# Optimization experiments

Hardware: AMD Instinct MI355X
Metric: run time of the kernel (lower is better)

## Reference

```python
import jax, jax.numpy as jnp
import numpy as np

D_MODEL, D_FF, RANK = 1024, 4096, 256
B, S = 4, 4096


def setup_inputs() -> dict:
    key = jax.random.key(0)
    ks = jax.random.split(key, 7)
    return {
        "x":  jax.random.normal(ks[0], (B, S, D_MODEL), dtype=jnp.float32),
        "U1": jax.random.normal(ks[1], (D_MODEL, RANK), dtype=jnp.float32) * 0.02,
        "V1": jax.random.normal(ks[2], (RANK, D_FF), dtype=jnp.float32) * 0.02,
        "b1": jnp.zeros((D_FF,), dtype=jnp.float32),
        "U2": jax.random.normal(ks[3], (D_FF, RANK), dtype=jnp.float32) * 0.02,
        "V2": jax.random.normal(ks[4], (RANK, D_MODEL), dtype=jnp.float32) * 0.02,
        "b2": jnp.zeros((D_MODEL,), dtype=jnp.float32),
    }


def reference(x, U1, V1, b1, U2, V2, b2):
    # P = x @ U1  -> low-rank projection [B, S, rank]
    P = jnp.einsum("bsd,dr->bsr", x, U1)
    # H = gelu(P @ V1 + b1)  -> [B, S, d_ff] (the intermediate the flash kernel tiles over)
    H = jax.nn.gelu(jnp.einsum("bsr,rf->bsf", P, V1) + b1)
    # Q = H @ U2 -> [B, S, rank]; out = Q @ V2 + b2 -> [B, S, d_model]
    Q = jnp.einsum("bsf,fr->bsr", H, U2)
    return jnp.einsum("bsr,rd->bsd", Q, V2) + b2
```

## Files before the change

### kernel.cpp

```cpp
#include <hip/hip_runtime.h>
#include <hip/hip_bf16.h>


typedef __attribute__((ext_vector_type(8))) short bfrag8;
typedef __attribute__((ext_vector_type(4))) float fx4;
typedef __attribute__((ext_vector_type(4))) unsigned short usx4;

#define D_MODEL 1024
#define D_FF    4096
#define RANK    256
#define NROWS   16384
#define PSTR    264
#define XSTR    136

__device__ __forceinline__ unsigned short f2b(float f) {
  __hip_bfloat16 h = __float2bfloat16(f);
  unsigned short u; __builtin_memcpy(&u, &h, 2); return u;
}
__device__ __forceinline__ float b2f(unsigned short u) {
  union { unsigned u; float f; } v; v.u = ((unsigned)u) << 16; return v.f;
}

__device__ __forceinline__ float gelu_tanh(float x) {
  float x2 = x * x;
  float inner = __builtin_fmaf(0.044715f * x2, x, x);
  float e = __builtin_amdgcn_exp2f(2.302118885f * inner);
  float t = __builtin_fmaf(-2.0f, __builtin_amdgcn_rcpf(1.0f + e), 1.0f);
  float hx = 0.5f * x;
  return __builtin_fmaf(hx, t, hx);
}

__device__ __forceinline__ void gl_lds16(const unsigned short* g, unsigned short* l) {
  __builtin_amdgcn_global_load_lds(
      (const __attribute__((address_space(1))) unsigned int*)g,
      (__attribute__((address_space(3))) unsigned int*)l, 16, 0, 0);
}

__global__ void packall(const float* __restrict__ U1, const float* __restrict__ V1,
                        const float* __restrict__ U2, const float* __restrict__ V2,
                        unsigned short* __restrict__ u1t, unsigned short* __restrict__ v1c,
                        unsigned short* __restrict__ u2c, unsigned short* __restrict__ v2t) {
  __shared__ float t[32][33];
  const int b = blockIdx.x;
  const int tx = threadIdx.x & 31, ty = threadIdx.x >> 5;
  if (b < 256) {
    int c0 = (b & 7) * 32, r0 = (b >> 3) * 32;
#pragma unroll
    for (int i = 0; i < 32; i += 8)
      t[ty + i][tx] = U1[(size_t)(r0 + ty + i) * RANK + c0 + tx];
    __syncthreads();
#pragma unroll
    for (int i = 0; i < 32; i += 8)
      u1t[(size_t)(c0 + ty + i) * D_MODEL + r0 + tx] = f2b(t[tx][ty + i]);
  } else if (b < 1280) {
    int tt = b - 256;
    int f0 = (tt & 127) * 32, k0 = (tt >> 7) * 32;
#pragma unroll
    for (int i = 0; i < 32; i += 8)
      t[ty + i][tx] = V1[(size_t)(k0 + ty + i) * D_FF + f0 + tx];
    __syncthreads();
#pragma unroll
    for (int i = 0; i < 32; i += 8) {
      int f = ty + i;
      v1c[(size_t)(f0 + f) * RANK + ((k0 + tx) ^ ((f & 7) << 3))] = f2b(t[tx][f]);
    }
  } else if (b < 2304) {
    int tt = b - 1280;
    int f0 = (tt & 127) * 32, r0 = (tt >> 7) * 32, cg = tt & 127;
#pragma unroll
    for (int i = 0; i < 32; i += 8)
      t[ty + i][tx] = U2[(size_t)(f0 + ty + i) * RANK + r0 + tx];
    __syncthreads();
#pragma unroll
    for (int i = 0; i < 32; i += 8) {
      int r2l = ty + i;
      int s = tx ^ (((r2l >> 1) & 3) << 3);
      int fl = (((s & 7) >= 4) ? 16 : 0) + 4 * (s >> 3) + (s & 3);
      u2c[(size_t)cg * 8192 + (size_t)(r0 + r2l) * 32 + tx] = f2b(t[fl][r2l]);
    }
  } else {
    int tt = b - 2304;
    int c0 = (tt & 31) * 32, r0 = (tt >> 5) * 32;
#pragma unroll
    for (int i = 0; i < 32; i += 8)
      t[ty + i][tx] = V2[(size_t)(r0 + ty + i) * D_MODEL + c0 + tx];
    __syncthreads();
#pragma unroll
    for (int i = 0; i < 32; i += 8)
      v2t[(size_t)(c0 + ty + i) * RANK + r0 + tx] = f2b(t[tx][ty + i]);
  }
}

__global__ __launch_bounds__(256, 4) void pgemm(
    const float* __restrict__ x, const unsigned short* __restrict__ u1t,
    unsigned short* __restrict__ P)
{
  __shared__ unsigned short xs[32 * XSTR];
  const int tid = threadIdx.x;
  const int w = tid >> 6, lane = tid & 63, lo = lane & 15, hi = lane >> 4;
  const size_t gr0 = (size_t)blockIdx.x * 32;

  fx4 acc[2][4];
#pragma unroll
  for (int mt = 0; mt < 2; ++mt)
#pragma unroll
    for (int nt = 0; nt < 4; ++nt) acc[mt][nt] = fx4{0.f, 0.f, 0.f, 0.f};

  for (int d0 = 0; d0 < D_MODEL; d0 += 128) {
    __syncthreads();
#pragma unroll
    for (int it = 0; it < 4; ++it) {
      int idx = it * 256 + tid;
      int r = idx >> 5, c = (idx & 31) << 2;
      fx4 v = *(const fx4*)(x + (gr0 + r) * D_MODEL + d0 + c);
      usx4 bv; bv[0] = f2b(v[0]); bv[1] = f2b(v[1]); bv[2] = f2b(v[2]); bv[3] = f2b(v[3]);
      *(usx4*)(xs + r * XSTR + c) = bv;
    }
    __syncthreads();
#pragma unroll
    for (int ks = 0; ks < 128; ks += 32) {
      bfrag8 a[2], b[4];
#pragma unroll
      for (int mt = 0; mt < 2; ++mt)
        a[mt] = *(const bfrag8*)(xs + (16 * mt + lo) * XSTR + ks + hi * 8);
#pragma unroll
      for (int nt = 0; nt < 4; ++nt)
        b[nt] = *(const bfrag8*)(u1t + (size_t)(w * 64 + nt * 16 + lo) * D_MODEL + d0 + ks + hi * 8);
#pragma unroll
      for (int mt = 0; mt < 2; ++mt)
#pragma unroll
        for (int nt = 0; nt < 4; ++nt)
          acc[mt][nt] = __builtin_amdgcn_mfma_f32_16x16x32_bf16(a[mt], b[nt], acc[mt][nt], 0, 0, 0);
    }
  }
#pragma unroll
  for (int mt = 0; mt < 2; ++mt)
#pragma unroll
    for (int nt = 0; nt < 4; ++nt)
#pragma unroll
      for (int r = 0; r < 4; ++r)
        P[(gr0 + 16 * mt + 4 * hi + r) * RANK + w * 64 + nt * 16 + lo] = f2b(acc[mt][nt][r]);
}

__global__ __launch_bounds__(256, 2) void hqgemm(
    const unsigned short* __restrict__ P,
    const unsigned short* __restrict__ v1c,
    const float* __restrict__ b1,
    const unsigned short* __restrict__ u2c,
    unsigned short* __restrict__ qpart,
    int F)
{
  __shared__ unsigned short v1s[2][32 * 256];
  __shared__ unsigned short u2s[2][256 * 32];
  __shared__ float b1s[1024];

  const int tid = threadIdx.x;
  const int w = tid >> 6, lane = tid & 63, lo = lane & 15, hi = lane >> 4;

  const int bid = blockIdx.x;
  const int j = bid % F;
  const int rb = bid / F;
  const int fspan = D_FF / F;
  const int fbase = j * fspan;
  const int nchunk = fspan / 32;
  const int rowstart = rb * 128 + w * 32;

  bfrag8 pf[2][8];
#pragma unroll
  for (int rg = 0; rg < 2; ++rg)
#pragma unroll
    for (int ks = 0; ks < 8; ++ks)
      pf[rg][ks] = *(const bfrag8*)(P + (size_t)(rowstart + 16 * rg + lo) * RANK + ks * 32 + hi * 8);
  for (int i = tid; i < fspan; i += 256) b1s[i] = b1[fbase + i];
  __syncthreads();

  fx4 qacc[2][16];
#pragma unroll
  for (int rg = 0; rg < 2; ++rg)
#pragma unroll
    for (int nt = 0; nt < 16; ++nt) qacc[rg][nt] = fx4{0.f, 0.f, 0.f, 0.f};

  const int vswz = (lo & 7) << 3;
  const int qoff = (hi * 8) ^ (((lo >> 1) & 3) << 3);
  const int vbase = lo * 256;

#define HQ_STAGE(C, B) do {                                                    \
    const unsigned short* vsrc_ = v1c + (size_t)(fbase + (C) * 32) * 256;      \
    const unsigned short* usrc_ = u2c + (size_t)((fbase >> 5) + (C)) * 8192;   \
    _Pragma("unroll")                                                          \
    for (int p = 0; p < 4; ++p) {                                              \
      int off_ = tid * 8 + p * 2048;                                           \
      gl_lds16(vsrc_ + off_, &v1s[B][off_]);                                   \
      gl_lds16(usrc_ + off_, &u2s[B][off_]);                                   \
    } } while (0)

  HQ_STAGE(0, 0);
  if (nchunk > 1) HQ_STAGE(1, 1);

  int cur = 0;
  for (int c = 0; c < nchunk; ++c) {
    if (c + 1 < nchunk) asm volatile("s_waitcnt vmcnt(8)" ::: "memory");
    else                asm volatile("s_waitcnt vmcnt(0)" ::: "memory");
    asm volatile("s_barrier" ::: "memory");
    __builtin_amdgcn_sched_barrier(0);

    const unsigned short* vb = v1s[cur];
    const unsigned short* ub = u2s[cur];

    fx4 hacc[2][2];
#pragma unroll
    for (int t = 0; t < 2; ++t)
#pragma unroll
      for (int rg = 0; rg < 2; ++rg) hacc[t][rg] = fx4{0.f, 0.f, 0.f, 0.f};
    __builtin_amdgcn_s_setprio(1);
#pragma unroll
    for (int ks = 0; ks < 8; ++ks) {
      int ko = (ks * 32 + hi * 8) ^ vswz;
      bfrag8 vE = *(const bfrag8*)(vb + vbase + ko);
      bfrag8 vO = *(const bfrag8*)(vb + vbase + 4096 + ko);
      hacc[0][0] = __builtin_amdgcn_mfma_f32_16x16x32_bf16(vE, pf[0][ks], hacc[0][0], 0, 0, 0);
      hacc[0][1] = __builtin_amdgcn_mfma_f32_16x16x32_bf16(vE, pf[1][ks], hacc[0][1], 0, 0, 0);
      hacc[1][0] = __builtin_amdgcn_mfma_f32_16x16x32_bf16(vO, pf[0][ks], hacc[1][0], 0, 0, 0);
      hacc[1][1] = __builtin_amdgcn_mfma_f32_16x16x32_bf16(vO, pf[1][ks], hacc[1][1], 0, 0, 0);
    }
    __builtin_amdgcn_s_setprio(0);

    fx4 bE = *(const fx4*)(&b1s[c * 32 + 4 * hi]);
    fx4 bO = *(const fx4*)(&b1s[c * 32 + 16 + 4 * hi]);
    bfrag8 bq0, bq1;
#pragma unroll
    for (int r = 0; r < 4; ++r) {
      bq0[r]     = (short)f2b(gelu_tanh(hacc[0][0][r] + bE[r]));
      bq0[r + 4] = (short)f2b(gelu_tanh(hacc[1][0][r] + bO[r]));
      bq1[r]     = (short)f2b(gelu_tanh(hacc[0][1][r] + bE[r]));
      bq1[r + 4] = (short)f2b(gelu_tanh(hacc[1][1][r] + bO[r]));
    }

    __builtin_amdgcn_s_setprio(1);
#pragma unroll
    for (int nt = 0; nt < 16; ++nt) {
      bfrag8 qa = *(const bfrag8*)(ub + (16 * nt + lo) * 32 + qoff);
      qacc[0][nt] = __builtin_amdgcn_mfma_f32_16x16x32_bf16(qa, bq0, qacc[0][nt], 0, 0, 0);
      qacc[1][nt] = __builtin_amdgcn_mfma_f32_16x16x32_bf16(qa, bq1, qacc[1][nt], 0, 0, 0);
    }
    __builtin_amdgcn_s_setprio(0);

    __builtin_amdgcn_sched_barrier(0);
    asm volatile("s_barrier" ::: "memory");
    if (c + 2 < nchunk) HQ_STAGE(c + 2, cur);
    cur ^= 1;
  }
#undef HQ_STAGE

  unsigned short* qp = qpart + (size_t)j * NROWS * RANK;
#pragma unroll
  for (int rg = 0; rg < 2; ++rg) {
    size_t row = (size_t)(rowstart + 16 * rg + lo);
#pragma unroll
    for (int nt = 0; nt < 16; ++nt) {
      usx4 qv;
      qv[0] = f2b(qacc[rg][nt][0]); qv[1] = f2b(qacc[rg][nt][1]);
      qv[2] = f2b(qacc[rg][nt][2]); qv[3] = f2b(qacc[rg][nt][3]);
      *(usx4*)(qp + row * RANK + 16 * nt + 4 * hi) = qv;
    }
  }
}

__global__ __launch_bounds__(512, 4) void ogemm(
    const unsigned short* __restrict__ qpart, int F,
    const unsigned short* __restrict__ v2t,
    const float* __restrict__ b2,
    float* __restrict__ out)
{
  __shared__ unsigned short Qs[64 * PSTR];
  const int tid = threadIdx.x;
  const int w = tid >> 6, lane = tid & 63, lo = lane & 15, hi = lane >> 4;
  const int wm = w >> 2, wn = w & 3;
  const size_t gr0 = (size_t)blockIdx.x * 64;
  const int n0 = blockIdx.y * 512 + wn * 128;

#pragma unroll
  for (int it = 0; it < 8; ++it) {
    int idx = it * 512 + tid;
    int r = idx >> 6, c = (idx & 63) << 2;
    float s0 = 0.f, s1 = 0.f, s2 = 0.f, s3 = 0.f;
    for (int jj = 0; jj < F; ++jj) {
      usx4 q = *(const usx4*)(qpart + (size_t)jj * NROWS * RANK + (gr0 + r) * RANK + c);
      s0 += b2f(q[0]); s1 += b2f(q[1]); s2 += b2f(q[2]); s3 += b2f(q[3]);
    }
    usx4 bv; bv[0] = f2b(s0); bv[1] = f2b(s1); bv[2] = f2b(s2); bv[3] = f2b(s3);
    *(usx4*)(Qs + r * PSTR + c) = bv;
  }
  __syncthreads();

  fx4 acc[2][8];
#pragma unroll
  for (int mt = 0; mt < 2; ++mt)
#pragma unroll
    for (int nt = 0; nt < 8; ++nt) acc[mt][nt] = fx4{0.f, 0.f, 0.f, 0.f};

#pragma unroll
  for (int ks = 0; ks < RANK; ks += 32) {
    bfrag8 a[2], b[8];
#pragma unroll
    for (int mt = 0; mt < 2; ++mt)
      a[mt] = *(const bfrag8*)(Qs + (wm * 32 + 16 * mt + lo) * PSTR + ks + hi * 8);
#pragma unroll
    for (int nt = 0; nt < 8; ++nt)
      b[nt] = *(const bfrag8*)(v2t + (size_t)(n0 + nt * 16 + lo) * RANK + ks + hi * 8);
#pragma unroll
    for (int mt = 0; mt < 2; ++mt)
#pragma unroll
      for (int nt = 0; nt < 8; ++nt)
        acc[mt][nt] = __builtin_amdgcn_mfma_f32_16x16x32_bf16(a[mt], b[nt], acc[mt][nt], 0, 0, 0);
  }

#pragma unroll
  for (int nt = 0; nt < 8; ++nt) {
    int col = n0 + nt * 16 + lo;
    float bias = b2[col];
#pragma unroll
    for (int mt = 0; mt < 2; ++mt)
#pragma unroll
      for (int r = 0; r < 4; ++r)
        out[(gr0 + wm * 32 + 16 * mt + 4 * hi + r) * D_MODEL + col] = acc[mt][nt][r] + bias;
  }
}

extern "C" void kernel_launch(void* const* d_in, const int* in_sizes, int n_in,
                              void* d_out, int out_size, void* d_ws, size_t ws_size,
                              hipStream_t stream) {
  const float* x  = (const float*)d_in[0];
  const float* U1 = (const float*)d_in[1];
  const float* V1 = (const float*)d_in[2];
  const float* b1 = (const float*)d_in[3];
  const float* U2 = (const float*)d_in[4];
  const float* V2 = (const float*)d_in[5];
  const float* b2 = (const float*)d_in[6];
  float* out = (float*)d_out;

  unsigned short* ws16 = (unsigned short*)d_ws;
  unsigned short* u1t = ws16;
  unsigned short* v1c = u1t + (size_t)RANK * D_MODEL;
  unsigned short* u2c = v1c + (size_t)D_FF * RANK;
  unsigned short* v2t = u2c + (size_t)RANK * D_FF;
  unsigned short* Pbf = v2t + (size_t)D_MODEL * RANK;
  unsigned short* qpart = Pbf + (size_t)NROWS * RANK;

  size_t fixed_bytes = 2ull * ((size_t)RANK * D_MODEL + (size_t)D_FF * RANK +
                               (size_t)RANK * D_FF + (size_t)D_MODEL * RANK +
                               (size_t)NROWS * RANK);
  size_t qb = (size_t)NROWS * RANK * 2;
  int F = (ws_size >= fixed_bytes + 4 * qb) ? 4 : 2;

  packall<<<2560, 256, 0, stream>>>(U1, V1, U2, V2, u1t, v1c, u2c, v2t);
  pgemm<<<NROWS / 32, 256, 0, stream>>>(x, u1t, Pbf);
  hqgemm<<<(NROWS / 128) * F, 256, 0, stream>>>(Pbf, v1c, b1, u2c, qpart, F);
  ogemm<<<dim3(NROWS / 64, D_MODEL / 512), 512, 0, stream>>>(qpart, F, v2t, b2, out);
}
```

Baseline: 179.9 us.

## Warp-specialize hqgemm into producer H waves and consumer Q waves via LDS

Splits hqgemm into 512-thread blocks where four waves compute the P·V1 tile plus GELU and write the bf16 activations to a double-buffered LDS area, while four other waves load U2 tiles and run the H·U2 MFMAs one chunk behind. This separates the two GEMM phases so they overlap across wave groups instead of running back to back in each wave. It also removes the U2 swizzle in packall and in the LDS reads, rewrites GELU as x·sigmoid form, and fixes the F split at 2. In exchange it doubles threads per block, adds per-chunk barriers and full vmcnt waits, and the unswizzled U2 layout may cause LDS bank conflicts.

```diff
diff --git a/kernel.cpp b/kernel.cpp
--- a/kernel.cpp
+++ b/kernel.cpp
@@ -24,10 +24,8 @@
 __device__ __forceinline__ float gelu_tanh(float x) {
   float x2 = x * x;
   float inner = __builtin_fmaf(0.044715f * x2, x, x);
-  float e = __builtin_amdgcn_exp2f(2.302118885f * inner);
-  float t = __builtin_fmaf(-2.0f, __builtin_amdgcn_rcpf(1.0f + e), 1.0f);
-  float hx = 0.5f * x;
-  return __builtin_fmaf(hx, t, hx);
+  float e = __builtin_amdgcn_exp2f(-2.302118885f * inner);
+  return x * __builtin_amdgcn_rcpf(1.0f + e);
 }
 
 __device__ __forceinline__ void gl_lds16(const unsigned short* g, unsigned short* l) {
@@ -74,9 +72,7 @@
 #pragma unroll
     for (int i = 0; i < 32; i += 8) {
       int r2l = ty + i;
-      int s = tx ^ (((r2l >> 1) & 3) << 3);
-      int fl = (((s & 7) >= 4) ? 16 : 0) + 4 * (s >> 3) + (s & 3);
-      u2c[(size_t)cg * 8192 + (size_t)(r0 + r2l) * 32 + tx] = f2b(t[fl][r2l]);
+      u2c[(size_t)cg * 8192 + (size_t)(r0 + r2l) * 32 + tx] = f2b(t[tx][r2l]);
     }
   } else {
     int tt = b - 2304;
@@ -142,7 +138,7 @@
         P[(gr0 + 16 * mt + 4 * hi + r) * RANK + w * 64 + nt * 16 + lo] = f2b(acc[mt][nt][r]);
 }
 
-__global__ __launch_bounds__(256, 2) void hqgemm(
+__global__ __launch_bounds__(512, 2) void hqgemm(
     const unsigned short* __restrict__ P,
     const unsigned short* __restrict__ v1c,
     const float* __restrict__ b1,
@@ -152,116 +148,129 @@
 {
   __shared__ unsigned short v1s[2][32 * 256];
   __shared__ unsigned short u2s[2][256 * 32];
-  __shared__ float b1s[1024];
+  __shared__ unsigned short bqs[2][128 * 32];
 
   const int tid = threadIdx.x;
   const int w = tid >> 6, lane = tid & 63, lo = lane & 15, hi = lane >> 4;
+  const bool isH = (w < 4);
+  const int hw = w & 3;
+  const int stid = tid & 255;
 
   const int bid = blockIdx.x;
-  const int j = bid % F;
+  const int j = bid & (F - 1);
   const int rb = bid / F;
   const int fspan = D_FF / F;
   const int fbase = j * fspan;
   const int nchunk = fspan / 32;
-  const int rowstart = rb * 128 + w * 32;
-
-  bfrag8 pf[2][8];
-#pragma unroll
-  for (int rg = 0; rg < 2; ++rg)
-#pragma unroll
-    for (int ks = 0; ks < 8; ++ks)
-      pf[rg][ks] = *(const bfrag8*)(P + (size_t)(rowstart + 16 * rg + lo) * RANK + ks * 32 + hi * 8);
-  for (int i = tid; i < fspan; i += 256) b1s[i] = b1[fbase + i];
-  __syncthreads();
-
-  fx4 qacc[2][16];
-#pragma unroll
-  for (int rg = 0; rg < 2; ++rg)
-#pragma unroll
-    for (int nt = 0; nt < 16; ++nt) qacc[rg][nt] = fx4{0.f, 0.f, 0.f, 0.f};
+  const int rowstart = rb * 128 + hw * 32;
 
   const int vswz = (lo & 7) << 3;
-  const int qoff = (hi * 8) ^ (((lo >> 1) & 3) << 3);
   const int vbase = lo * 256;
 
-#define HQ_STAGE(C, B) do {                                                    \
-    const unsigned short* vsrc_ = v1c + (size_t)(fbase + (C) * 32) * 256;      \
-    const unsigned short* usrc_ = u2c + (size_t)((fbase >> 5) + (C)) * 8192;   \
+#define STAGE_V(C, B) do {                                                     \
+    const unsigned short* s_ = v1c + (size_t)(fbase + (C) * 32) * 256;         \
     _Pragma("unroll")                                                          \
     for (int p = 0; p < 4; ++p) {                                              \
-      int off_ = tid * 8 + p * 2048;                                           \
-      gl_lds16(vsrc_ + off_, &v1s[B][off_]);                                   \
-      gl_lds16(usrc_ + off_, &u2s[B][off_]);                                   \
+      int o_ = stid * 8 + p * 2048;                                            \
+      gl_lds16(s_ + o_, &v1s[B][o_]);                                          \
     } } while (0)
-
-  HQ_STAGE(0, 0);
-  if (nchunk > 1) HQ_STAGE(1, 1);
-
-  int cur = 0;
-  for (int c = 0; c < nchunk; ++c) {
-    if (c + 1 < nchunk) asm volatile("s_waitcnt vmcnt(8)" ::: "memory");
-    else                asm volatile("s_waitcnt vmcnt(0)" ::: "memory");
+#define STAGE_U(C, B) do {                                                     \
+    const unsigned short* s_ = u2c + (size_t)((fbase >> 5) + (C)) * 8192;      \
+    _Pragma("unroll")                                                          \
+    for (int p = 0; p < 4; ++p) {                                              \
+      int o_ = stid * 8 + p * 2048;                                            \
+      gl_lds16(s_ + o_, &u2s[B][o_]);                                          \
+    } } while (0)
+
+  bfrag8 pf[2][8];
+  fx4 qacc[2][16];
+  if (isH) {
+#pragma unroll
+    for (int rg = 0; rg < 2; ++rg)
+#pragma unroll
+      for (int ks = 0; ks < 8; ++ks)
+        pf[rg][ks] = *(const bfrag8*)(P + (size_t)(rowstart + 16 * rg + lo) * RANK + ks * 32 + hi * 8);
+    STAGE_V(0, 0);
+    asm volatile("s_waitcnt vmcnt(0)" ::: "memory");
+  } else {
+#pragma unroll
+    for (int rg = 0; rg < 2; ++rg)
+#pragma unroll
+      for (int nt = 0; nt < 16; ++nt) qacc[rg][nt] = fx4{0.f, 0.f, 0.f, 0.f};
+  }
+
+  for (int i = 0; i <= nchunk; ++i) {
     asm volatile("s_barrier" ::: "memory");
-    __builtin_amdgcn_sched_barrier(0);
-
-    const unsigned short* vb = v1s[cur];
-    const unsigned short* ub = u2s[cur];
-
-    fx4 hacc[2][2];
-#pragma unroll
-    for (int t = 0; t < 2; ++t)
-#pragma unroll
-      for (int rg = 0; rg < 2; ++rg) hacc[t][rg] = fx4{0.f, 0.f, 0.f, 0.f};
-    __builtin_amdgcn_s_setprio(1);
-#pragma unroll
-    for (int ks = 0; ks < 8; ++ks) {
-      int ko = (ks * 32 + hi * 8) ^ vswz;
-      bfrag8 vE = *(const bfrag8*)(vb + vbase + ko);
-      bfrag8 vO = *(const bfrag8*)(vb + vbase + 4096 + ko);
-      hacc[0][0] = __builtin_amdgcn_mfma_f32_16x16x32_bf16(vE, pf[0][ks], hacc[0][0], 0, 0, 0);
-      hacc[0][1] = __builtin_amdgcn_mfma_f32_16x16x32_bf16(vE, pf[1][ks], hacc[0][1], 0, 0, 0);
-      hacc[1][0] = __builtin_amdgcn_mfma_f32_16x16x32_bf16(vO, pf[0][ks], hacc[1][0], 0, 0, 0);
-      hacc[1][1] = __builtin_amdgcn_mfma_f32_16x16x32_bf16(vO, pf[1][ks], hacc[1][1], 0, 0, 0);
-    }
-    __builtin_amdgcn_s_setprio(0);
-
-    fx4 bE = *(const fx4*)(&b1s[c * 32 + 4 * hi]);
-    fx4 bO = *(const fx4*)(&b1s[c * 32 + 16 + 4 * hi]);
-    bfrag8 bq0, bq1;
-#pragma unroll
-    for (int r = 0; r < 4; ++r) {
-      bq0[r]     = (short)f2b(gelu_tanh(hacc[0][0][r] + bE[r]));
-      bq0[r + 4] = (short)f2b(gelu_tanh(hacc[1][0][r] + bO[r]));
-      bq1[r]     = (short)f2b(gelu_tanh(hacc[0][1][r] + bE[r]));
-      bq1[r + 4] = (short)f2b(gelu_tanh(hacc[1][1][r] + bO[r]));
-    }
-
-    __builtin_amdgcn_s_setprio(1);
-#pragma unroll
-    for (int nt = 0; nt < 16; ++nt) {
-      bfrag8 qa = *(const bfrag8*)(ub + (16 * nt + lo) * 32 + qoff);
-      qacc[0][nt] = __builtin_amdgcn_mfma_f32_16x16x32_bf16(qa, bq0, qacc[0][nt], 0, 0, 0);
-      qacc[1][nt] = __builtin_amdgcn_mfma_f32_16x16x32_bf16(qa, bq1, qacc[1][nt], 0, 0, 0);
-    }
-    __builtin_amdgcn_s_setprio(0);
-
-    __builtin_amdgcn_sched_barrier(0);
-    asm volatile("s_barrier" ::: "memory");
-    if (c + 2 < nchunk) HQ_STAGE(c + 2, cur);
-    cur ^= 1;
-  }
-#undef HQ_STAGE
-
-  unsigned short* qp = qpart + (size_t)j * NROWS * RANK;
-#pragma unroll
-  for (int rg = 0; rg < 2; ++rg) {
-    size_t row = (size_t)(rowstart + 16 * rg + lo);
-#pragma unroll
-    for (int nt = 0; nt < 16; ++nt) {
-      usx4 qv;
-      qv[0] = f2b(qacc[rg][nt][0]); qv[1] = f2b(qacc[rg][nt][1]);
-      qv[2] = f2b(qacc[rg][nt][2]); qv[3] = f2b(qacc[rg][nt][3]);
-      *(usx4*)(qp + row * RANK + 16 * nt + 4 * hi) = qv;
+    if (isH) {
+      if (i < nchunk) {
+        const int f0g = fbase + i * 32;
+        if (i + 1 < nchunk) STAGE_V(i + 1, (i + 1) & 1);
+        fx4 bE = *(const fx4*)(b1 + f0g + 4 * hi);
+        fx4 bO = *(const fx4*)(b1 + f0g + 16 + 4 * hi);
+
+        const unsigned short* vb = v1s[i & 1];
+        fx4 hacc[2][2];
+#pragma unroll
+        for (int t = 0; t < 2; ++t)
+#pragma unroll
+          for (int rg = 0; rg < 2; ++rg) hacc[t][rg] = fx4{0.f, 0.f, 0.f, 0.f};
+#pragma unroll
+        for (int ks = 0; ks < 8; ++ks) {
+          int ko = (ks * 32 + hi * 8) ^ vswz;
+          bfrag8 vE = *(const bfrag8*)(vb + vbase + ko);
+          bfrag8 vO = *(const bfrag8*)(vb + vbase + 4096 + ko);
+          hacc[0][0] = __builtin_amdgcn_mfma_f32_16x16x32_bf16(vE, pf[0][ks], hacc[0][0], 0, 0, 0);
+          hacc[0][1] = __builtin_amdgcn_mfma_f32_16x16x32_bf16(vE, pf[1][ks], hacc[0][1], 0, 0, 0);
+          hacc[1][0] = __builtin_amdgcn_mfma_f32_16x16x32_bf16(vO, pf[0][ks], hacc[1][0], 0, 0, 0);
+          hacc[1][1] = __builtin_amdgcn_mfma_f32_16x16x32_bf16(vO, pf[1][ks], hacc[1][1], 0, 0, 0);
+        }
+#pragma unroll
+        for (int rg = 0; rg < 2; ++rg) {
+          usx4 p0, p1;
+#pragma unroll
+          for (int r = 0; r < 4; ++r) {
+            p0[r] = f2b(gelu_tanh(hacc[0][rg][r] + bE[r]));
+            p1[r] = f2b(gelu_tanh(hacc[1][rg][r] + bO[r]));
+          }
+          int row = hw * 32 + 16 * rg + lo;
+          *(usx4*)(&bqs[i & 1][row * 32 + 4 * hi])      = p0;
+          *(usx4*)(&bqs[i & 1][row * 32 + 16 + 4 * hi]) = p1;
+        }
+        asm volatile("s_waitcnt lgkmcnt(0)" ::: "memory");
+        asm volatile("s_waitcnt vmcnt(0)" ::: "memory");
+      }
+    } else {
+      if (i < nchunk) STAGE_U(i, i & 1);
+      if (i >= 1) {
+        const unsigned short* ub = u2s[(i - 1) & 1];
+        const unsigned short* bb = bqs[(i - 1) & 1];
+        bfrag8 bq0 = *(const bfrag8*)(bb + (hw * 32 + lo) * 32 + hi * 8);
+        bfrag8 bq1 = *(const bfrag8*)(bb + (hw * 32 + 16 + lo) * 32 + hi * 8);
+#pragma unroll
+        for (int nt = 0; nt < 16; ++nt) {
+          bfrag8 qa = *(const bfrag8*)(ub + (16 * nt + lo) * 32 + hi * 8);
+          qacc[0][nt] = __builtin_amdgcn_mfma_f32_16x16x32_bf16(qa, bq0, qacc[0][nt], 0, 0, 0);
+          qacc[1][nt] = __builtin_amdgcn_mfma_f32_16x16x32_bf16(qa, bq1, qacc[1][nt], 0, 0, 0);
+        }
+      }
+      asm volatile("s_waitcnt vmcnt(0)" ::: "memory");
+    }
+  }
+#undef STAGE_V
+#undef STAGE_U
+
+  if (!isH) {
+    unsigned short* qp = qpart + (size_t)j * NROWS * RANK;
+#pragma unroll
+    for (int rg = 0; rg < 2; ++rg) {
+      size_t row = (size_t)(rowstart + 16 * rg + lo);
+#pragma unroll
+      for (int nt = 0; nt < 16; ++nt) {
+        usx4 qv;
+        qv[0] = f2b(qacc[rg][nt][0]); qv[1] = f2b(qacc[rg][nt][1]);
+        qv[2] = f2b(qacc[rg][nt][2]); qv[3] = f2b(qacc[rg][nt][3]);
+        *(usx4*)(qp + row * RANK + 16 * nt + 4 * hi) = qv;
+      }
     }
   }
 }
@@ -347,14 +356,10 @@
   unsigned short* Pbf = v2t + (size_t)D_MODEL * RANK;
   unsigned short* qpart = Pbf + (size_t)NROWS * RANK;
 
-  size_t fixed_bytes = 2ull * ((size_t)RANK * D_MODEL + (size_t)D_FF * RANK +
-                               (size_t)RANK * D_FF + (size_t)D_MODEL * RANK +
-                               (size_t)NROWS * RANK);
-  size_t qb = (size_t)NROWS * RANK * 2;
-  int F = (ws_size >= fixed_bytes + 4 * qb) ? 4 : 2;
+  const int F = 2;
 
   packall<<<2560, 256, 0, stream>>>(U1, V1, U2, V2, u1t, v1c, u2c, v2t);
   pgemm<<<NROWS / 32, 256, 0, stream>>>(x, u1t, Pbf);
-  hqgemm<<<(NROWS / 128) * F, 256, 0, stream>>>(Pbf, v1c, b1, u2c, qpart, F);
+  hqgemm<<<(NROWS / 128) * F, 512, 0, stream>>>(Pbf, v1c, b1, u2c, qpart, F);
   ogemm<<<dim3(NROWS / 64, D_MODEL / 512), 512, 0, stream>>>(qpart, F, v2t, b2, out);
 }
```

Result: slower. 203.0 us (+12.8%).

## Software-pipeline H and Q stages with split V/U staging and simplify GELU

Applied to the files above, without the earlier changes.

Restructures the fused H->Q loop so the H-GEMM and GELU for chunk c run after the Q-GEMM of chunk c-1. This lets the MFMA work of both stages interleave, and V1 and U2 tiles are now staged separately on different schedules. The GELU is rewritten algebraically as x*sigmoid(2*inner), which saves a few ALU ops. The cost is one barrier per iteration with a full vmcnt(0) wait, which may expose load latency that the old partial wait hid, and the two-buffer indexing becomes more complex.

```diff
diff --git a/kernel.cpp b/kernel.cpp
--- a/kernel.cpp
+++ b/kernel.cpp
@@ -24,10 +24,8 @@
 __device__ __forceinline__ float gelu_tanh(float x) {
   float x2 = x * x;
   float inner = __builtin_fmaf(0.044715f * x2, x, x);
-  float e = __builtin_amdgcn_exp2f(2.302118885f * inner);
-  float t = __builtin_fmaf(-2.0f, __builtin_amdgcn_rcpf(1.0f + e), 1.0f);
-  float hx = 0.5f * x;
-  return __builtin_fmaf(hx, t, hx);
+  float e = __builtin_amdgcn_exp2f(-2.302118885f * inner);
+  return x * __builtin_amdgcn_rcpf(1.0f + e);
 }
 
 __device__ __forceinline__ void gl_lds16(const unsigned short* g, unsigned short* l) {
@@ -184,29 +182,32 @@
   const int qoff = (hi * 8) ^ (((lo >> 1) & 3) << 3);
   const int vbase = lo * 256;
 
-#define HQ_STAGE(C, B) do {                                                    \
-    const unsigned short* vsrc_ = v1c + (size_t)(fbase + (C) * 32) * 256;      \
-    const unsigned short* usrc_ = u2c + (size_t)((fbase >> 5) + (C)) * 8192;   \
+#define STAGE_V(C, B) do {                                                     \
+    const unsigned short* s_ = v1c + (size_t)(fbase + (C) * 32) * 256;         \
     _Pragma("unroll")                                                          \
     for (int p = 0; p < 4; ++p) {                                              \
-      int off_ = tid * 8 + p * 2048;                                           \
-      gl_lds16(vsrc_ + off_, &v1s[B][off_]);                                   \
-      gl_lds16(usrc_ + off_, &u2s[B][off_]);                                   \
+      int o_ = tid * 8 + p * 2048;                                             \
+      gl_lds16(s_ + o_, &v1s[B][o_]);                                          \
     } } while (0)
-
-  HQ_STAGE(0, 0);
-  if (nchunk > 1) HQ_STAGE(1, 1);
-
-  int cur = 0;
-  for (int c = 0; c < nchunk; ++c) {
-    if (c + 1 < nchunk) asm volatile("s_waitcnt vmcnt(8)" ::: "memory");
-    else                asm volatile("s_waitcnt vmcnt(0)" ::: "memory");
-    asm volatile("s_barrier" ::: "memory");
-    __builtin_amdgcn_sched_barrier(0);
-
-    const unsigned short* vb = v1s[cur];
-    const unsigned short* ub = u2s[cur];
-
+#define STAGE_U(C, B) do {                                                     \
+    const unsigned short* s_ = u2c + (size_t)((fbase >> 5) + (C)) * 8192;      \
+    _Pragma("unroll")                                                          \
+    for (int p = 0; p < 4; ++p) {                                              \
+      int o_ = tid * 8 + p * 2048;                                             \
+      gl_lds16(s_ + o_, &u2s[B][o_]);                                          \
+    } } while (0)
+
+  bfrag8 bq0, bq1;
+
+  STAGE_V(0, 0);
+  STAGE_U(0, 0);
+  if (nchunk > 1) STAGE_V(1, 1);
+  asm volatile("s_waitcnt vmcnt(8)" ::: "memory");
+  asm volatile("s_barrier" ::: "memory");
+  __builtin_amdgcn_sched_barrier(0);
+
+  {
+    const unsigned short* vb = v1s[0];
     fx4 hacc[2][2];
 #pragma unroll
     for (int t = 0; t < 2; ++t)
@@ -224,10 +225,8 @@
       hacc[1][1] = __builtin_amdgcn_mfma_f32_16x16x32_bf16(vO, pf[1][ks], hacc[1][1], 0, 0, 0);
     }
     __builtin_amdgcn_s_setprio(0);
-
-    fx4 bE = *(const fx4*)(&b1s[c * 32 + 4 * hi]);
-    fx4 bO = *(const fx4*)(&b1s[c * 32 + 16 + 4 * hi]);
-    bfrag8 bq0, bq1;
+    fx4 bE = *(const fx4*)(&b1s[4 * hi]);
+    fx4 bO = *(const fx4*)(&b1s[16 + 4 * hi]);
 #pragma unroll
     for (int r = 0; r < 4; ++r) {
       bq0[r]     = (short)f2b(gelu_tanh(hacc[0][0][r] + bE[r]));
@@ -235,7 +234,16 @@
       bq1[r]     = (short)f2b(gelu_tanh(hacc[0][1][r] + bE[r]));
       bq1[r + 4] = (short)f2b(gelu_tanh(hacc[1][1][r] + bO[r]));
     }
-
+  }
+
+  for (int c = 1; c <= nchunk; ++c) {
+    asm volatile("s_waitcnt vmcnt(0)" ::: "memory");
+    asm volatile("s_barrier" ::: "memory");
+    __builtin_amdgcn_sched_barrier(0);
+    if (c < nchunk) STAGE_U(c, c & 1);
+    if (c + 1 < nchunk) STAGE_V(c + 1, (c + 1) & 1);
+
+    const unsigned short* ub = u2s[(c - 1) & 1];
     __builtin_amdgcn_s_setprio(1);
 #pragma unroll
     for (int nt = 0; nt < 16; ++nt) {
@@ -243,14 +251,40 @@
       qacc[0][nt] = __builtin_amdgcn_mfma_f32_16x16x32_bf16(qa, bq0, qacc[0][nt], 0, 0, 0);
       qacc[1][nt] = __builtin_amdgcn_mfma_f32_16x16x32_bf16(qa, bq1, qacc[1][nt], 0, 0, 0);
     }
-    __builtin_amdgcn_s_setprio(0);
-
-    __builtin_amdgcn_sched_barrier(0);
-    asm volatile("s_barrier" ::: "memory");
-    if (c + 2 < nchunk) HQ_STAGE(c + 2, cur);
-    cur ^= 1;
-  }
-#undef HQ_STAGE
+
+    if (c < nchunk) {
+      const unsigned short* vb = v1s[c & 1];
+      fx4 hacc[2][2];
+#pragma unroll
+      for (int t = 0; t < 2; ++t)
+#pragma unroll
+        for (int rg = 0; rg < 2; ++rg) hacc[t][rg] = fx4{0.f, 0.f, 0.f, 0.f};
+#pragma unroll
+      for (int ks = 0; ks < 8; ++ks) {
+        int ko = (ks * 32 + hi * 8) ^ vswz;
+        bfrag8 vE = *(const bfrag8*)(vb + vbase + ko);
+        bfrag8 vO = *(const bfrag8*)(vb + vbase + 4096 + ko);
+        hacc[0][0] = __builtin_amdgcn_mfma_f32_16x16x32_bf16(vE, pf[0][ks], hacc[0][0], 0, 0, 0);
+        hacc[0][1] = __builtin_amdgcn_mfma_f32_16x16x32_bf16(vE, pf[1][ks], hacc[0][1], 0, 0, 0);
+        hacc[1][0] = __builtin_amdgcn_mfma_f32_16x16x32_bf16(vO, pf[0][ks], hacc[1][0], 0, 0, 0);
+        hacc[1][1] = __builtin_amdgcn_mfma_f32_16x16x32_bf16(vO, pf[1][ks], hacc[1][1], 0, 0, 0);
+      }
+      __builtin_amdgcn_s_setprio(0);
+      fx4 bE = *(const fx4*)(&b1s[c * 32 + 4 * hi]);
+      fx4 bO = *(const fx4*)(&b1s[c * 32 + 16 + 4 * hi]);
+#pragma unroll
+      for (int r = 0; r < 4; ++r) {
+        bq0[r]     = (short)f2b(gelu_tanh(hacc[0][0][r] + bE[r]));
+        bq0[r + 4] = (short)f2b(gelu_tanh(hacc[1][0][r] + bO[r]));
+        bq1[r]     = (short)f2b(gelu_tanh(hacc[0][1][r] + bE[r]));
+        bq1[r + 4] = (short)f2b(gelu_tanh(hacc[1][1][r] + bO[r]));
+      }
+    } else {
+      __builtin_amdgcn_s_setprio(0);
+    }
+  }
+#undef STAGE_V
+#undef STAGE_U
 
   unsigned short* qp = qpart + (size_t)j * NROWS * RANK;
 #pragma unroll
```

Result: no change. 176.7 us (-1.8%).
